# Optimization experiments

Measured on AMD Instinct MI355X. Metric: run time of the kernel, lower is better.

Reference implementation:

```python
import jax, jax.numpy as jnp
import numpy as np

TEMPERATURE = 0.5
EPS = 1e-12  # matches torch F.normalize default eps


def _l2_normalize(x):
    norm = jnp.sqrt(jnp.sum(x * x, axis=-1, keepdims=True))
    return x / jnp.maximum(norm, EPS)


def setup_inputs() -> dict:
    key = jax.random.key(0)
    k1, k2 = jax.random.split(key)
    B, C, D = 64, 512, 256
    visual_features = jax.random.normal(k1, (B, C, D), dtype=jnp.float32)
    text_embeddings = jax.random.normal(k2, (B, C, D), dtype=jnp.float32)
    return {"visual_features": visual_features, "text_embeddings": text_embeddings}


def reference(visual_features, text_embeddings):
    v = _l2_normalize(visual_features)   # (B, C, D)
    t = _l2_normalize(text_embeddings)   # (B, C, D)
    # positive: diagonal similarity per class
    sim_pos = jnp.einsum('bcd,bcd->bc', v, t)
    positive = jnp.exp(sim_pos / TEMPERATURE)            # (B, C)
    # full BxCxC similarity matrix
    all_sim = jnp.exp(jnp.einsum('bcd,bkd->bck', v, t) / TEMPERATURE)
    negative = jnp.sum(all_sim, axis=-1) - positive      # (B, C)
    loss = -jnp.log(positive / (positive + negative))
    return jnp.mean(loss)
```

## Files before the change

kernel.cpp:

```cpp
#include <hip/hip_runtime.h>
#include <hip/hip_bf16.h>

#define BB 64
#define CC 512
#define DD 256

typedef __attribute__((ext_vector_type(8))) short bf16x8;
typedef __attribute__((ext_vector_type(4))) float f32x4;
typedef unsigned int u32;

#define SWZ(r) (((r) & 7) << 4)

__device__ inline short f2bf(float f) {
    union { __hip_bfloat16 h; short s; } cv;
    cv.h = __float2bfloat16(f);
    return cv.s;
}

__global__ __launch_bounds__(256) void norm_rows(const float* __restrict__ in,
                                                 unsigned short* __restrict__ out) {
    const int row  = blockIdx.x * 4 + (threadIdx.x >> 6);
    const int lane = threadIdx.x & 63;
    const float4 x = reinterpret_cast<const float4*>(in)[(size_t)row * 64 + lane];
    float ss = x.x * x.x + x.y * x.y + x.z * x.z + x.w * x.w;
#pragma unroll
    for (int off = 32; off; off >>= 1) ss += __shfl_xor(ss, off);
    const float r = 1.0f / fmaxf(sqrtf(ss), 1e-12f);
    ushort4 o;
    o.x = (unsigned short)f2bf(x.x * r);
    o.y = (unsigned short)f2bf(x.y * r);
    o.z = (unsigned short)f2bf(x.z * r);
    o.w = (unsigned short)f2bf(x.w * r);
    reinterpret_cast<ushort4*>(out)[(size_t)row * 64 + lane] = o;
}

__global__ __launch_bounds__(256, 4) void gemm_loss(const float* __restrict__ V,
                                                    const unsigned short* __restrict__ Tn,
                                                    float* __restrict__ partials) {
    __shared__ char ldsb[32768];
    __shared__ float vred[128];
    __shared__ float dred[128];

    const int i0 = blockIdx.x;
    const int b  = (i0 & 7) * 8 + ((i0 >> 3) & 7);
    const int rb = i0 >> 6;

    const int tid  = threadIdx.x;
    const int lane = tid & 63;
    const int wave = tid >> 6;
    const int wr   = wave >> 1;
    const int wc   = wave & 1;
    const int g    = lane >> 4;
    const int ln   = lane & 15;

    const float* gV = V + (size_t)b * (CC * DD) + (size_t)rb * 64 * DD;
    const char*  gT = reinterpret_cast<const char*>(Tn + (size_t)b * (CC * DD));

    {
        const int rrow  = tid >> 3;
        const int ecolB = (tid & 7) * 64;
#pragma unroll
        for (int p = 0; p < 2; ++p) {
            const float4* src =
                reinterpret_cast<const float4*>(gV + (size_t)(p * 32 + rrow) * DD) + (tid & 7) * 8;
            float4 x[8];
#pragma unroll
            for (int q = 0; q < 8; ++q) x[q] = src[q];
            float ss = 0.f;
#pragma unroll
            for (int q = 0; q < 8; ++q)
                ss += x[q].x * x[q].x + x[q].y * x[q].y + x[q].z * x[q].z + x[q].w * x[q].w;
            ss += __shfl_xor(ss, 1);
            ss += __shfl_xor(ss, 2);
            ss += __shfl_xor(ss, 4);
            const float rinv = 1.0f / fmaxf(sqrtf(ss), 1e-12f);
            const int row = p * 32 + rrow;
            char* dstrow  = ldsb + row * 512;
            const int sw  = SWZ(row);
#pragma unroll
            for (int q2 = 0; q2 < 4; ++q2) {
                const float4 v0 = x[2 * q2], v1 = x[2 * q2 + 1];
                bf16x8 o;
                o[0] = f2bf(v0.x * rinv); o[1] = f2bf(v0.y * rinv);
                o[2] = f2bf(v0.z * rinv); o[3] = f2bf(v0.w * rinv);
                o[4] = f2bf(v1.x * rinv); o[5] = f2bf(v1.y * rinv);
                o[6] = f2bf(v1.z * rinv); o[7] = f2bf(v1.w * rinv);
                *reinterpret_cast<bf16x8*>(dstrow + ((ecolB + q2 * 16) ^ sw)) = o;
            }
        }
    }
    __syncthreads();

    bf16x8 a[2][8];
#pragma unroll
    for (int i = 0; i < 2; ++i) {
        const int row  = wr * 32 + i * 16 + ln;
        const char* rp = ldsb + row * 512;
        const int sw   = SWZ(row);
#pragma unroll
        for (int kk = 0; kk < 8; ++kk)
            a[i][kk] = *reinterpret_cast<const bf16x8*>(rp + ((kk * 64 + g * 16) ^ sw));
    }
    __syncthreads();

#pragma unroll
    for (int t0 = 0; t0 < 2; ++t0) {
        const char* gtile = gT + (size_t)t0 * 32 * 512;
        char* dst = ldsb + t0 * 16384 + wave * 4096;
#pragma unroll
        for (int r2 = 0; r2 < 4; ++r2) {
            const int L  = r2 * 1024 + (lane << 4);
            const int lr = L >> 9, inrow = L & 511;
            __builtin_amdgcn_global_load_lds(
                (const u32*)(gtile + (size_t)(wave * 8 + lr) * 512 + (inrow ^ SWZ(lr))),
                (u32*)(dst + r2 * 1024), 16, 0, 0);
        }
    }

    float rs[2][4];
    float dg[2][4];
#pragma unroll
    for (int i = 0; i < 2; ++i)
#pragma unroll
        for (int r = 0; r < 4; ++r) { rs[i][r] = 0.f; dg[i][r] = 0.f; }

    for (int t = 0; t < 16; ++t) {
        if (t < 15) asm volatile("s_waitcnt vmcnt(4)" ::: "memory");
        else        asm volatile("s_waitcnt vmcnt(0)" ::: "memory");
        __builtin_amdgcn_s_barrier();
        __builtin_amdgcn_sched_barrier(0);

        const char* rp = ldsb + (t & 1) * 16384 + (wc * 16 + ln) * 512;
        const int sw   = SWZ(ln);
        f32x4 acc[2] = {(f32x4){0.f, 0.f, 0.f, 0.f}, (f32x4){0.f, 0.f, 0.f, 0.f}};
        __builtin_amdgcn_s_setprio(1);
#pragma unroll
        for (int kk = 0; kk < 8; ++kk) {
            const bf16x8 bb = *reinterpret_cast<const bf16x8*>(rp + ((kk * 64 + g * 16) ^ sw));
            acc[0] = __builtin_amdgcn_mfma_f32_16x16x32_bf16(a[0][kk], bb, acc[0], 0, 0, 0);
            acc[1] = __builtin_amdgcn_mfma_f32_16x16x32_bf16(a[1][kk], bb, acc[1], 0, 0, 0);
        }
        __builtin_amdgcn_s_setprio(0);

        const int gcol = t * 32 + wc * 16 + ln;
#pragma unroll
        for (int i = 0; i < 2; ++i) {
            const int grow = rb * 64 + wr * 32 + i * 16 + g * 4;
#pragma unroll
            for (int r = 0; r < 4; ++r) {
                const float s2 = acc[i][r] * 2.0f;
                rs[i][r] += __expf(s2);
                if (gcol == grow + r) dg[i][r] += s2;
            }
        }

        __builtin_amdgcn_s_barrier();
        __builtin_amdgcn_sched_barrier(0);
        if (t < 14) {
            const char* gtile = gT + (size_t)(t + 2) * 32 * 512;
            char* dst = ldsb + (t & 1) * 16384 + wave * 4096;
#pragma unroll
            for (int r2 = 0; r2 < 4; ++r2) {
                const int L  = r2 * 1024 + (lane << 4);
                const int lr = L >> 9, inrow = L & 511;
                __builtin_amdgcn_global_load_lds(
                    (const u32*)(gtile + (size_t)(wave * 8 + lr) * 512 + (inrow ^ SWZ(lr))),
                    (u32*)(dst + r2 * 1024), 16, 0, 0);
            }
        }
    }

#pragma unroll
    for (int i = 0; i < 2; ++i)
#pragma unroll
        for (int r = 0; r < 4; ++r) {
            float v = rs[i][r];
            float d = dg[i][r];
#pragma unroll
            for (int m = 1; m < 16; m <<= 1) {
                v += __shfl_xor(v, m);
                d += __shfl_xor(d, m);
            }
            if (ln == 0) {
                const int rl = wr * 32 + i * 16 + g * 4 + r;
                vred[rl * 2 + wc] = v;
                dred[rl * 2 + wc] = d;
            }
        }
    __syncthreads();

    if (tid < 64) {
        const float vv = vred[tid * 2] + vred[tid * 2 + 1];
        const float dd = dred[tid * 2] + dred[tid * 2 + 1];
        float lsum = logf(vv) - dd;
#pragma unroll
        for (int m = 1; m < 64; m <<= 1) lsum += __shfl_xor(lsum, m);
        if (tid == 0) partials[i0] = lsum;
    }
}

__global__ __launch_bounds__(256) void final_reduce(const float* __restrict__ partials,
                                                    float* __restrict__ out) {
    const int t = threadIdx.x;
    float v = partials[t] + partials[t + 256];
#pragma unroll
    for (int m = 1; m < 64; m <<= 1) v += __shfl_xor(v, m);
    __shared__ float red[4];
    if ((t & 63) == 0) red[t >> 6] = v;
    __syncthreads();
    if (t == 0) out[0] = (red[0] + red[1] + red[2] + red[3]) * (1.0f / 32768.0f);
}

extern "C" void kernel_launch(void* const* d_in, const int* in_sizes, int n_in,
                              void* d_out, int out_size, void* d_ws, size_t ws_size,
                              hipStream_t stream) {
    const float* vis = (const float*)d_in[0];
    const float* txt = (const float*)d_in[1];

    unsigned short* Tn = (unsigned short*)d_ws;
    float* partials    = (float*)((char*)d_ws + (size_t)BB * CC * DD * 2);
    float* out         = (float*)d_out;

    norm_rows<<<8192, 256, 0, stream>>>(txt, Tn);
    gemm_loss<<<512, 256, 0, stream>>>(vis, Tn, partials);
    final_reduce<<<1, 256, 0, stream>>>(partials, out);
}
```

Baseline: 40.47 us.

## Use 512-thread blocks with 128-row tiles and triple-buffered T staging

Each block now handles 128 rows of V with 8 waves instead of 64 rows with 4, halving the grid to 256 blocks so each T tile loaded into LDS is shared by twice as many rows. T staging moves to a 3-stage ring buffer, and the next load is issued right after the barrier at the top of each iteration, which removes the second barrier per iteration. The cost is a larger LDS footprint (64KB plus small buffers), fewer blocks than CUs on a large GPU, and an extra block-level reduction step.

```diff
diff --git a/kernel.cpp b/kernel.cpp
--- a/kernel.cpp
+++ b/kernel.cpp
@@ -34,16 +34,18 @@
     reinterpret_cast<ushort4*>(out)[(size_t)row * 64 + lane] = o;
 }
 
-__global__ __launch_bounds__(256, 4) void gemm_loss(const float* __restrict__ V,
+__global__ __launch_bounds__(512, 2) void gemm_loss(const float* __restrict__ V,
                                                     const unsigned short* __restrict__ Tn,
                                                     float* __restrict__ partials) {
-    __shared__ char ldsb[32768];
-    __shared__ float vred[128];
-    __shared__ float dred[128];
-
-    const int i0 = blockIdx.x;
-    const int b  = (i0 & 7) * 8 + ((i0 >> 3) & 7);
-    const int rb = i0 >> 6;
+    __shared__ char ldsb[65536];
+    __shared__ float vred[256];
+    __shared__ float dred[256];
+    __shared__ float red2[2];
+
+    const int i0    = blockIdx.x;
+    const int inner = i0 & 63;
+    const int b     = (inner & 7) * 8 + (inner >> 3);
+    const int rb    = i0 >> 6;
 
     const int tid  = threadIdx.x;
     const int lane = tid & 63;
@@ -53,7 +55,7 @@
     const int g    = lane >> 4;
     const int ln   = lane & 15;
 
-    const float* gV = V + (size_t)b * (CC * DD) + (size_t)rb * 64 * DD;
+    const float* gV = V + (size_t)b * (CC * DD) + (size_t)rb * 128 * DD;
     const char*  gT = reinterpret_cast<const char*>(Tn + (size_t)b * (CC * DD));
 
     {
@@ -61,8 +63,9 @@
         const int ecolB = (tid & 7) * 64;
 #pragma unroll
         for (int p = 0; p < 2; ++p) {
+            const int row = p * 64 + rrow;
             const float4* src =
-                reinterpret_cast<const float4*>(gV + (size_t)(p * 32 + rrow) * DD) + (tid & 7) * 8;
+                reinterpret_cast<const float4*>(gV + (size_t)row * DD) + (tid & 7) * 8;
             float4 x[8];
 #pragma unroll
             for (int q = 0; q < 8; ++q) x[q] = src[q];
@@ -74,9 +77,8 @@
             ss += __shfl_xor(ss, 2);
             ss += __shfl_xor(ss, 4);
             const float rinv = 1.0f / fmaxf(sqrtf(ss), 1e-12f);
-            const int row = p * 32 + rrow;
-            char* dstrow  = ldsb + row * 512;
-            const int sw  = SWZ(row);
+            char* dstrow = ldsb + row * 512;
+            const int sw = SWZ(row);
 #pragma unroll
             for (int q2 = 0; q2 < 4; ++q2) {
                 const float4 v0 = x[2 * q2], v1 = x[2 * q2 + 1];
@@ -103,19 +105,22 @@
     }
     __syncthreads();
 
-#pragma unroll
-    for (int t0 = 0; t0 < 2; ++t0) {
-        const char* gtile = gT + (size_t)t0 * 32 * 512;
-        char* dst = ldsb + t0 * 16384 + wave * 4096;
-#pragma unroll
-        for (int r2 = 0; r2 < 4; ++r2) {
-            const int L  = r2 * 1024 + (lane << 4);
-            const int lr = L >> 9, inrow = L & 511;
+    auto stage = [&](int t) {
+        const char* gtile = gT + (size_t)t * 16384;
+        char* dst = ldsb + (t % 3) * 16384 + wave * 2048;
+#pragma unroll
+        for (int r2 = 0; r2 < 2; ++r2) {
+            const int L   = r2 * 1024 + (lane << 4);
+            const int lr  = L >> 9;
+            const int row = wave * 4 + lr;
+            const int inrow = L & 511;
             __builtin_amdgcn_global_load_lds(
-                (const u32*)(gtile + (size_t)(wave * 8 + lr) * 512 + (inrow ^ SWZ(lr))),
+                (const u32*)(gtile + (size_t)row * 512 + (inrow ^ SWZ(row))),
                 (u32*)(dst + r2 * 1024), 16, 0, 0);
         }
-    }
+    };
+    stage(0);
+    stage(1);
 
     float rs[2][4];
     float dg[2][4];
@@ -125,12 +130,13 @@
         for (int r = 0; r < 4; ++r) { rs[i][r] = 0.f; dg[i][r] = 0.f; }
 
     for (int t = 0; t < 16; ++t) {
-        if (t < 15) asm volatile("s_waitcnt vmcnt(4)" ::: "memory");
+        if (t < 15) asm volatile("s_waitcnt vmcnt(2)" ::: "memory");
         else        asm volatile("s_waitcnt vmcnt(0)" ::: "memory");
         __builtin_amdgcn_s_barrier();
         __builtin_amdgcn_sched_barrier(0);
-
-        const char* rp = ldsb + (t & 1) * 16384 + (wc * 16 + ln) * 512;
+        if (t < 14) stage(t + 2);
+
+        const char* rp = ldsb + (t % 3) * 16384 + (wc * 16 + ln) * 512;
         const int sw   = SWZ(ln);
         f32x4 acc[2] = {(f32x4){0.f, 0.f, 0.f, 0.f}, (f32x4){0.f, 0.f, 0.f, 0.f}};
         __builtin_amdgcn_s_setprio(1);
@@ -145,7 +151,7 @@
         const int gcol = t * 32 + wc * 16 + ln;
 #pragma unroll
         for (int i = 0; i < 2; ++i) {
-            const int grow = rb * 64 + wr * 32 + i * 16 + g * 4;
+            const int grow = rb * 128 + wr * 32 + i * 16 + g * 4;
 #pragma unroll
             for (int r = 0; r < 4; ++r) {
                 const float s2 = acc[i][r] * 2.0f;
@@ -153,21 +159,6 @@
                 if (gcol == grow + r) dg[i][r] += s2;
             }
         }
-
-        __builtin_amdgcn_s_barrier();
-        __builtin_amdgcn_sched_barrier(0);
-        if (t < 14) {
-            const char* gtile = gT + (size_t)(t + 2) * 32 * 512;
-            char* dst = ldsb + (t & 1) * 16384 + wave * 4096;
-#pragma unroll
-            for (int r2 = 0; r2 < 4; ++r2) {
-                const int L  = r2 * 1024 + (lane << 4);
-                const int lr = L >> 9, inrow = L & 511;
-                __builtin_amdgcn_global_load_lds(
-                    (const u32*)(gtile + (size_t)(wave * 8 + lr) * 512 + (inrow ^ SWZ(lr))),
-                    (u32*)(dst + r2 * 1024), 16, 0, 0);
-            }
-        }
     }
 
 #pragma unroll
@@ -189,20 +180,22 @@
         }
     __syncthreads();
 
-    if (tid < 64) {
+    if (tid < 128) {
         const float vv = vred[tid * 2] + vred[tid * 2 + 1];
         const float dd = dred[tid * 2] + dred[tid * 2 + 1];
         float lsum = logf(vv) - dd;
 #pragma unroll
         for (int m = 1; m < 64; m <<= 1) lsum += __shfl_xor(lsum, m);
-        if (tid == 0) partials[i0] = lsum;
-    }
+        if (lane == 0) red2[wave] = lsum;
+    }
+    __syncthreads();
+    if (tid == 0) partials[i0] = red2[0] + red2[1];
 }
 
 __global__ __launch_bounds__(256) void final_reduce(const float* __restrict__ partials,
                                                     float* __restrict__ out) {
     const int t = threadIdx.x;
-    float v = partials[t] + partials[t + 256];
+    float v = partials[t];
 #pragma unroll
     for (int m = 1; m < 64; m <<= 1) v += __shfl_xor(v, m);
     __shared__ float red[4];
@@ -222,6 +215,6 @@
     float* out         = (float*)d_out;
 
     norm_rows<<<8192, 256, 0, stream>>>(txt, Tn);
-    gemm_loss<<<512, 256, 0, stream>>>(vis, Tn, partials);
+    gemm_loss<<<256, 512, 0, stream>>>(vis, Tn, partials);
     final_reduce<<<1, 256, 0, stream>>>(partials, out);
 }
```

Result: no change. 39.70 us (-1.9%).
